# Kernel tuning notes

Hardware: AMD Instinct MI355X
Metric: run time of the kernel (lower is better)

Reference implementation:

```python
import jax, jax.numpy as jnp
import numpy as np

TEMPERATURE = 0.2
EPS = 1e-12  # matches torch F.normalize eps


def _l2_normalize(x):
    n = jnp.linalg.norm(x, axis=-1, keepdims=True)
    return x / jnp.maximum(n, EPS)


def setup_inputs() -> dict:
    key = jax.random.key(0)
    k1, k2 = jax.random.split(key)
    B, D = 8192, 256
    return {
        "user_embeddings": jax.random.normal(k1, (B, D), dtype=jnp.float32),
        "positive_item_embeddings": jax.random.normal(k2, (B, D), dtype=jnp.float32),
    }


def reference(user_embeddings, positive_item_embeddings):
    # all_item_embeddings=None branch: in-batch implicit negatives.
    u = _l2_normalize(user_embeddings)            # [B, D]
    p = _l2_normalize(positive_item_embeddings)   # [B, D]
    sim = jnp.einsum("bd,nd->bn", u, p) / TEMPERATURE  # [B, B]
    pos_sim = jnp.diagonal(sim)                   # [B]; equals the torch pos_sim
    # Original concatenates pos_sim[i] with the off-diagonal row entries and takes
    # logsumexp. Since the diagonal of sim IS pos_sim[i], that set equals the full
    # row, so loss_i = -pos_sim_i + logsumexp(sim[i, :]). Vectorized over the batch.
    lse = jax.nn.logsumexp(sim, axis=1)           # [B]
    return jnp.mean(lse - pos_sim)
```

## Files before the change

kernel.cpp:

```cpp
#include <hip/hip_runtime.h>
#include <hip/hip_bf16.h>

#define DDIM 256
#define NROWS 8192

typedef __attribute__((ext_vector_type(8))) __bf16 bf16x8;
typedef __attribute__((ext_vector_type(4))) float floatx4;

__device__ __forceinline__ void async16(const void* g, void* l) {
    __builtin_amdgcn_global_load_lds(
        (const __attribute__((address_space(1))) unsigned int*)g,
        (__attribute__((address_space(3))) unsigned int*)l,
        16, 0, 0);
}

__device__ __forceinline__ float fexp2(float x) {
    float r; asm("v_exp_f32 %0, %1" : "=v"(r) : "v"(x)); return r;
}

__global__ __launch_bounds__(256) void normalize_kernel(
    const float* __restrict__ U, const float* __restrict__ P,
    unsigned short* __restrict__ Un, unsigned short* __restrict__ Pn,
    float* __restrict__ possim, float* __restrict__ rowsum,
    float* __restrict__ out, int* __restrict__ counter)
{
    if (blockIdx.x == 0 && threadIdx.x == 0) { out[0] = 0.0f; counter[0] = 0; }
    const int lane = threadIdx.x & 63;
    const int row  = blockIdx.x * 4 + (threadIdx.x >> 6);
    const size_t base = (size_t)row * DDIM + lane * 4;
    const float4 u4 = *(const float4*)(U + base);
    const float4 p4 = *(const float4*)(P + base);
    float su = u4.x*u4.x + u4.y*u4.y + u4.z*u4.z + u4.w*u4.w;
    float sp = p4.x*p4.x + p4.y*p4.y + p4.z*p4.z + p4.w*p4.w;
    float up = u4.x*p4.x + u4.y*p4.y + u4.z*p4.z + u4.w*p4.w;
    #pragma unroll
    for (int d = 1; d < 64; d <<= 1) {
        su += __shfl_xor(su, d);
        sp += __shfl_xor(sp, d);
        up += __shfl_xor(up, d);
    }
    const float iu = rsqrtf(fmaxf(su, 1e-24f));
    const float ip = rsqrtf(fmaxf(sp, 1e-24f));
    if (lane == 0) {
        possim[row] = up * iu * ip;
        rowsum[row] = 0.0f;
    }
    union { ushort4 s4; __hip_bfloat16 h[4]; } cu, cp;
    cu.h[0] = __float2bfloat16(u4.x * iu); cu.h[1] = __float2bfloat16(u4.y * iu);
    cu.h[2] = __float2bfloat16(u4.z * iu); cu.h[3] = __float2bfloat16(u4.w * iu);
    cp.h[0] = __float2bfloat16(p4.x * ip); cp.h[1] = __float2bfloat16(p4.y * ip);
    cp.h[2] = __float2bfloat16(p4.z * ip); cp.h[3] = __float2bfloat16(p4.w * ip);
    *(ushort4*)(Un + base) = cu.s4;
    *(ushort4*)(Pn + base) = cp.s4;
}

__device__ __forceinline__ void stage8(const unsigned short* __restrict__ g,
                                       unsigned short* l, int wv, int lane)
{
    const int lrow = lane >> 5;
    const int gcol = lane & 31;
    const int r0 = wv * 8;
    #pragma unroll
    for (int j = 0; j < 4; ++j) {
        const int rb = r0 + j * 2;
        const int r  = rb + lrow;
        const int gg = gcol ^ (r & 7);
        async16(g + (size_t)r * DDIM + gg * 8, l + (size_t)rb * DDIM);
    }
}

__global__ __launch_bounds__(512, 2) void sim_exp_rowsum(
    const unsigned short* __restrict__ Un,
    const unsigned short* __restrict__ Pn,
    float* __restrict__ rowsum,
    const float* __restrict__ possim,
    int* __restrict__ counter,
    float* __restrict__ out)
{
    __shared__ __align__(16) unsigned short lds[65536];
    __shared__ float ws8[8];
    __shared__ int ticket_s;

    const int tid  = threadIdx.x;
    const int lane = tid & 63;
    const int wv   = tid >> 6;
    const int m = lane & 15;
    const int q = lane >> 4;

    const int stripe = blockIdx.x >> 3;
    const int oct    = blockIdx.x & 7;

    const unsigned short* Arow = Un + (size_t)(stripe * 256 + wv * 32 + m) * DDIM;
    bf16x8 afr[2][8];
    #pragma unroll
    for (int t = 0; t < 2; ++t)
        #pragma unroll
        for (int ks = 0; ks < 8; ++ks)
            afr[t][ks] = *(const bf16x8*)(Arow + t * 16 * DDIM + (ks * 4 + q) * 8);

    const int c10 = m & 3, c2 = (m >> 2) & 1;
    const unsigned bb0 = (unsigned)(m * 512 + ((q ^ c10) << 4) + ((0 ^ c2) << 6));
    const unsigned bb1 = (unsigned)(m * 512 + ((q ^ c10) << 4) + ((1 ^ c2) << 6));

    const unsigned short* Bglob = Pn + (size_t)(oct * 1024) * DDIM;
    float rowpart[2][4] = {{0.f, 0.f, 0.f, 0.f}, {0.f, 0.f, 0.f, 0.f}};

    stage8(Bglob,                  lds,         wv, lane);
    stage8(Bglob + 64 * DDIM,      lds + 16384, wv, lane);
    stage8(Bglob + 128 * DDIM,     lds + 32768, wv, lane);
    asm volatile("s_waitcnt vmcnt(0)" ::: "memory");
    __builtin_amdgcn_s_barrier();

#define LOADPH(BP, P, F)                                                     \
    do {                                                                     \
        F[0] = *(const bf16x8*)((BP) + bb0 + 0 * 8192 + (P) * 128);          \
        F[1] = *(const bf16x8*)((BP) + bb0 + 1 * 8192 + (P) * 128);          \
        F[2] = *(const bf16x8*)((BP) + bb0 + 2 * 8192 + (P) * 128);          \
        F[3] = *(const bf16x8*)((BP) + bb0 + 3 * 8192 + (P) * 128);          \
        F[4] = *(const bf16x8*)((BP) + bb1 + 0 * 8192 + (P) * 128);          \
        F[5] = *(const bf16x8*)((BP) + bb1 + 1 * 8192 + (P) * 128);          \
        F[6] = *(const bf16x8*)((BP) + bb1 + 2 * 8192 + (P) * 128);          \
        F[7] = *(const bf16x8*)((BP) + bb1 + 3 * 8192 + (P) * 128);          \
    } while (0)

#define MMAPH(P, F)                                                          \
    do {                                                                     \
        __builtin_amdgcn_s_setprio(1);                                       \
        _Pragma("unroll")                                                    \
        for (int n = 0; n < 4; ++n) {                                        \
            acc[0][n] = __builtin_amdgcn_mfma_f32_16x16x32_bf16(             \
                afr[0][2 * (P)], F[n], acc[0][n], 0, 0, 0);                  \
            acc[1][n] = __builtin_amdgcn_mfma_f32_16x16x32_bf16(             \
                afr[1][2 * (P)], F[n], acc[1][n], 0, 0, 0);                  \
            acc[0][n] = __builtin_amdgcn_mfma_f32_16x16x32_bf16(             \
                afr[0][2 * (P) + 1], F[n + 4], acc[0][n], 0, 0, 0);          \
            acc[1][n] = __builtin_amdgcn_mfma_f32_16x16x32_bf16(             \
                afr[1][2 * (P) + 1], F[n + 4], acc[1][n], 0, 0, 0);          \
        }                                                                    \
        __builtin_amdgcn_s_setprio(0);                                       \
    } while (0)

    for (int i = 0; i < 16; ++i) {
        if (i > 0) {
            if (i <= 13)      asm volatile("s_waitcnt vmcnt(8)" ::: "memory");
            else if (i == 14) asm volatile("s_waitcnt vmcnt(4)" ::: "memory");
            else              asm volatile("s_waitcnt vmcnt(0)" ::: "memory");
            __builtin_amdgcn_s_barrier();
        }
        if (i + 3 < 16)
            stage8(Bglob + (size_t)(i + 3) * 64 * DDIM,
                   lds + ((i + 3) & 3) * 16384, wv, lane);

        const char* Bp = (const char*)lds + (i & 3) * 32768;
        floatx4 acc[2][4];
        #pragma unroll
        for (int t = 0; t < 2; ++t)
            #pragma unroll
            for (int n = 0; n < 4; ++n)
                acc[t][n] = {0.0f, 0.0f, 0.0f, 0.0f};

        bf16x8 fA[8], fB[8];
        LOADPH(Bp, 0, fA);
        LOADPH(Bp, 1, fB);
        MMAPH(0, fA);
        LOADPH(Bp, 2, fA);
        MMAPH(1, fB);
        LOADPH(Bp, 3, fB);
        MMAPH(2, fA);
        MMAPH(3, fB);

        #pragma unroll
        for (int t = 0; t < 2; ++t)
            #pragma unroll
            for (int n = 0; n < 4; ++n)
                #pragma unroll
                for (int r = 0; r < 4; ++r)
                    rowpart[t][r] += fexp2(acc[t][n][r] * 7.2134752044448169f);
    }
#undef LOADPH
#undef MMAPH

    #pragma unroll
    for (int t = 0; t < 2; ++t) {
        #pragma unroll
        for (int r = 0; r < 4; ++r) {
            float s = rowpart[t][r];
            s += __shfl_xor(s, 1);
            s += __shfl_xor(s, 2);
            s += __shfl_xor(s, 4);
            s += __shfl_xor(s, 8);
            if (m == 0) {
                const int grow = stripe * 256 + wv * 32 + t * 16 + q * 4 + r;
                atomicAdd(&rowsum[grow], s);
            }
        }
    }

    __threadfence();
    __syncthreads();
    if (tid == 0)
        ticket_s = __hip_atomic_fetch_add(counter, 1, __ATOMIC_ACQ_REL,
                                          __HIP_MEMORY_SCOPE_AGENT);
    __syncthreads();
    if (ticket_s == 255) {
        float part = 0.0f;
        for (int i = tid; i < NROWS; i += 512) {
            const float rs = __hip_atomic_load(&rowsum[i], __ATOMIC_RELAXED,
                                               __HIP_MEMORY_SCOPE_AGENT);
            part += __logf(rs) - 5.0f * possim[i];
        }
        #pragma unroll
        for (int d = 1; d < 64; d <<= 1) part += __shfl_xor(part, d);
        if (lane == 0) ws8[wv] = part;
        __syncthreads();
        if (tid == 0) {
            float tot = 0.0f;
            #pragma unroll
            for (int w = 0; w < 8; ++w) tot += ws8[w];
            out[0] = tot * (1.0f / (float)NROWS);
        }
    }
}

extern "C" void kernel_launch(void* const* d_in, const int* in_sizes, int n_in,
                              void* d_out, int out_size, void* d_ws, size_t ws_size,
                              hipStream_t stream) {
    const float* U = (const float*)d_in[0];
    const float* P = (const float*)d_in[1];
    float* out = (float*)d_out;
    char* ws = (char*)d_ws;
    unsigned short* Un = (unsigned short*)ws;
    unsigned short* Pn = (unsigned short*)(ws + 4194304);
    float* rowsum = (float*)(ws + 8388608);
    float* possim = (float*)(ws + 8388608 + 32768);
    int* counter  = (int*)(ws + 8388608 + 65536);

    normalize_kernel<<<NROWS / 4, 256, 0, stream>>>(U, P, Un, Pn, possim, rowsum,
                                                    out, counter);
    sim_exp_rowsum<<<256, 512, 0, stream>>>(Un, Pn, rowsum, possim, counter, out);
}
```

Measured before the change: 144.6 us.

## Fuse normalization and similarity kernels into one cooperative kernel with grid sync

Moves the L2-normalize / bf16-convert / positive-similarity pass into the start of the main similarity kernel. Each of the 256 blocks normalizes 32 rows, then a cooperative grid-wide sync runs before the tiled bf16 matmul with its exp/rowsum reduction. This removes the second kernel launch and the gap between the two kernels. In exchange it adds a grid barrier and cooperative-launch overhead, and the normalize phase now runs on fewer, larger blocks.

```diff
diff --git a/kernel.cpp b/kernel.cpp
--- a/kernel.cpp
+++ b/kernel.cpp
@@ -1,5 +1,8 @@
 #include <hip/hip_runtime.h>
 #include <hip/hip_bf16.h>
+#include <hip/hip_cooperative_groups.h>
+
+namespace cg = cooperative_groups;
 
 #define DDIM 256
 #define NROWS 8192
@@ -16,42 +19,6 @@
 
 __device__ __forceinline__ float fexp2(float x) {
     float r; asm("v_exp_f32 %0, %1" : "=v"(r) : "v"(x)); return r;
-}
-
-__global__ __launch_bounds__(256) void normalize_kernel(
-    const float* __restrict__ U, const float* __restrict__ P,
-    unsigned short* __restrict__ Un, unsigned short* __restrict__ Pn,
-    float* __restrict__ possim, float* __restrict__ rowsum,
-    float* __restrict__ out, int* __restrict__ counter)
-{
-    if (blockIdx.x == 0 && threadIdx.x == 0) { out[0] = 0.0f; counter[0] = 0; }
-    const int lane = threadIdx.x & 63;
-    const int row  = blockIdx.x * 4 + (threadIdx.x >> 6);
-    const size_t base = (size_t)row * DDIM + lane * 4;
-    const float4 u4 = *(const float4*)(U + base);
-    const float4 p4 = *(const float4*)(P + base);
-    float su = u4.x*u4.x + u4.y*u4.y + u4.z*u4.z + u4.w*u4.w;
-    float sp = p4.x*p4.x + p4.y*p4.y + p4.z*p4.z + p4.w*p4.w;
-    float up = u4.x*p4.x + u4.y*p4.y + u4.z*p4.z + u4.w*p4.w;
-    #pragma unroll
-    for (int d = 1; d < 64; d <<= 1) {
-        su += __shfl_xor(su, d);
-        sp += __shfl_xor(sp, d);
-        up += __shfl_xor(up, d);
-    }
-    const float iu = rsqrtf(fmaxf(su, 1e-24f));
-    const float ip = rsqrtf(fmaxf(sp, 1e-24f));
-    if (lane == 0) {
-        possim[row] = up * iu * ip;
-        rowsum[row] = 0.0f;
-    }
-    union { ushort4 s4; __hip_bfloat16 h[4]; } cu, cp;
-    cu.h[0] = __float2bfloat16(u4.x * iu); cu.h[1] = __float2bfloat16(u4.y * iu);
-    cu.h[2] = __float2bfloat16(u4.z * iu); cu.h[3] = __float2bfloat16(u4.w * iu);
-    cp.h[0] = __float2bfloat16(p4.x * ip); cp.h[1] = __float2bfloat16(p4.y * ip);
-    cp.h[2] = __float2bfloat16(p4.z * ip); cp.h[3] = __float2bfloat16(p4.w * ip);
-    *(ushort4*)(Un + base) = cu.s4;
-    *(ushort4*)(Pn + base) = cp.s4;
 }
 
 __device__ __forceinline__ void stage8(const unsigned short* __restrict__ g,
@@ -69,13 +36,11 @@
     }
 }
 
-__global__ __launch_bounds__(512, 2) void sim_exp_rowsum(
-    const unsigned short* __restrict__ Un,
-    const unsigned short* __restrict__ Pn,
-    float* __restrict__ rowsum,
-    const float* __restrict__ possim,
-    int* __restrict__ counter,
-    float* __restrict__ out)
+__global__ __launch_bounds__(512, 2) void fused_loss(
+    const float* __restrict__ U, const float* __restrict__ P,
+    unsigned short* __restrict__ Un, unsigned short* __restrict__ Pn,
+    float* __restrict__ rowsum, float* __restrict__ possim,
+    int* __restrict__ counter, float* __restrict__ out)
 {
     __shared__ __align__(16) unsigned short lds[65536];
     __shared__ float ws8[8];
@@ -87,6 +52,44 @@
     const int m = lane & 15;
     const int q = lane >> 4;
 
+    if (blockIdx.x == 0 && tid == 0) counter[0] = 0;
+    {
+        const int r0 = blockIdx.x * 32 + wv * 4;
+        #pragma unroll
+        for (int rr = 0; rr < 4; ++rr) {
+            const int row = r0 + rr;
+            const size_t base = (size_t)row * DDIM + lane * 4;
+            const float4 u4 = *(const float4*)(U + base);
+            const float4 p4 = *(const float4*)(P + base);
+            float su = u4.x*u4.x + u4.y*u4.y + u4.z*u4.z + u4.w*u4.w;
+            float sp = p4.x*p4.x + p4.y*p4.y + p4.z*p4.z + p4.w*p4.w;
+            float up = u4.x*p4.x + u4.y*p4.y + u4.z*p4.z + u4.w*p4.w;
+            #pragma unroll
+            for (int d = 1; d < 64; d <<= 1) {
+                su += __shfl_xor(su, d);
+                sp += __shfl_xor(sp, d);
+                up += __shfl_xor(up, d);
+            }
+            const float iu = rsqrtf(fmaxf(su, 1e-24f));
+            const float ip = rsqrtf(fmaxf(sp, 1e-24f));
+            if (lane == 0) possim[row] = up * iu * ip;
+            union { ushort4 s4; __hip_bfloat16 h[4]; } cu, cp;
+            cu.h[0] = __float2bfloat16(u4.x * iu);
+            cu.h[1] = __float2bfloat16(u4.y * iu);
+            cu.h[2] = __float2bfloat16(u4.z * iu);
+            cu.h[3] = __float2bfloat16(u4.w * iu);
+            cp.h[0] = __float2bfloat16(p4.x * ip);
+            cp.h[1] = __float2bfloat16(p4.y * ip);
+            cp.h[2] = __float2bfloat16(p4.z * ip);
+            cp.h[3] = __float2bfloat16(p4.w * ip);
+            *(ushort4*)(Un + base) = cu.s4;
+            *(ushort4*)(Pn + base) = cp.s4;
+        }
+        if (tid < 32) rowsum[blockIdx.x * 32 + tid] = 0.0f;
+    }
+
+    cg::this_grid().sync();
+
     const int stripe = blockIdx.x >> 3;
     const int oct    = blockIdx.x & 7;
 
@@ -105,9 +108,9 @@
     const unsigned short* Bglob = Pn + (size_t)(oct * 1024) * DDIM;
     float rowpart[2][4] = {{0.f, 0.f, 0.f, 0.f}, {0.f, 0.f, 0.f, 0.f}};
 
-    stage8(Bglob,                  lds,         wv, lane);
-    stage8(Bglob + 64 * DDIM,      lds + 16384, wv, lane);
-    stage8(Bglob + 128 * DDIM,     lds + 32768, wv, lane);
+    stage8(Bglob,              lds,         wv, lane);
+    stage8(Bglob + 64 * DDIM,  lds + 16384, wv, lane);
+    stage8(Bglob + 128 * DDIM, lds + 32768, wv, lane);
     asm volatile("s_waitcnt vmcnt(0)" ::: "memory");
     __builtin_amdgcn_s_barrier();
 
@@ -235,7 +238,8 @@
     float* possim = (float*)(ws + 8388608 + 32768);
     int* counter  = (int*)(ws + 8388608 + 65536);
 
-    normalize_kernel<<<NROWS / 4, 256, 0, stream>>>(U, P, Un, Pn, possim, rowsum,
-                                                    out, counter);
-    sim_exp_rowsum<<<256, 512, 0, stream>>>(Un, Pn, rowsum, possim, counter, out);
-}
+    void* args[] = {(void*)&U, (void*)&P, (void*)&Un, (void*)&Pn,
+                    (void*)&rowsum, (void*)&possim, (void*)&counter, (void*)&out};
+    hipLaunchCooperativeKernel((const void*)fused_loss, dim3(256), dim3(512),
+                               args, 0, stream);
+}
```

Result: slower. 186.3 us (+28.9%).

## Load B fragments directly from global memory instead of staging through LDS

Applied to the files above, without the earlier changes.

Removes the LDS staging ring buffer, the async global-to-LDS copies and the per-iteration barriers. Each wave now reads its B fragments straight from global memory into registers, software-pipelined one phase ahead across iterations. This drops LDS traffic and block-wide synchronisation, but every wave independently fetches the same B tile. That multiplies global/L2 reads and exposes global latency to the MFMA loop.

```diff
diff --git a/kernel.cpp b/kernel.cpp
--- a/kernel.cpp
+++ b/kernel.cpp
@@ -6,13 +6,6 @@
 
 typedef __attribute__((ext_vector_type(8))) __bf16 bf16x8;
 typedef __attribute__((ext_vector_type(4))) float floatx4;
-
-__device__ __forceinline__ void async16(const void* g, void* l) {
-    __builtin_amdgcn_global_load_lds(
-        (const __attribute__((address_space(1))) unsigned int*)g,
-        (__attribute__((address_space(3))) unsigned int*)l,
-        16, 0, 0);
-}
 
 __device__ __forceinline__ float fexp2(float x) {
     float r; asm("v_exp_f32 %0, %1" : "=v"(r) : "v"(x)); return r;
@@ -54,21 +47,6 @@
     *(ushort4*)(Pn + base) = cp.s4;
 }
 
-__device__ __forceinline__ void stage8(const unsigned short* __restrict__ g,
-                                       unsigned short* l, int wv, int lane)
-{
-    const int lrow = lane >> 5;
-    const int gcol = lane & 31;
-    const int r0 = wv * 8;
-    #pragma unroll
-    for (int j = 0; j < 4; ++j) {
-        const int rb = r0 + j * 2;
-        const int r  = rb + lrow;
-        const int gg = gcol ^ (r & 7);
-        async16(g + (size_t)r * DDIM + gg * 8, l + (size_t)rb * DDIM);
-    }
-}
-
 __global__ __launch_bounds__(512, 2) void sim_exp_rowsum(
     const unsigned short* __restrict__ Un,
     const unsigned short* __restrict__ Pn,
@@ -77,7 +55,6 @@
     int* __restrict__ counter,
     float* __restrict__ out)
 {
-    __shared__ __align__(16) unsigned short lds[65536];
     __shared__ float ws8[8];
     __shared__ int ticket_s;
 
@@ -98,29 +75,24 @@
         for (int ks = 0; ks < 8; ++ks)
             afr[t][ks] = *(const bf16x8*)(Arow + t * 16 * DDIM + (ks * 4 + q) * 8);
 
-    const int c10 = m & 3, c2 = (m >> 2) & 1;
-    const unsigned bb0 = (unsigned)(m * 512 + ((q ^ c10) << 4) + ((0 ^ c2) << 6));
-    const unsigned bb1 = (unsigned)(m * 512 + ((q ^ c10) << 4) + ((1 ^ c2) << 6));
-
-    const unsigned short* Bglob = Pn + (size_t)(oct * 1024) * DDIM;
+    unsigned voff[2][4];
+    #pragma unroll
+    for (int par = 0; par < 2; ++par)
+        #pragma unroll
+        for (int n = 0; n < 4; ++n)
+            voff[par][n] = (unsigned)((n * 16 + m) * 512 + q * 16 + par * 64);
+
+    const char* Bbase = (const char*)(Pn + (size_t)(oct * 1024) * DDIM);
     float rowpart[2][4] = {{0.f, 0.f, 0.f, 0.f}, {0.f, 0.f, 0.f, 0.f}};
 
-    stage8(Bglob,                  lds,         wv, lane);
-    stage8(Bglob + 64 * DDIM,      lds + 16384, wv, lane);
-    stage8(Bglob + 128 * DDIM,     lds + 32768, wv, lane);
-    asm volatile("s_waitcnt vmcnt(0)" ::: "memory");
-    __builtin_amdgcn_s_barrier();
-
-#define LOADPH(BP, P, F)                                                     \
+#define LOADG(BS, P, F)                                                      \
     do {                                                                     \
-        F[0] = *(const bf16x8*)((BP) + bb0 + 0 * 8192 + (P) * 128);          \
-        F[1] = *(const bf16x8*)((BP) + bb0 + 1 * 8192 + (P) * 128);          \
-        F[2] = *(const bf16x8*)((BP) + bb0 + 2 * 8192 + (P) * 128);          \
-        F[3] = *(const bf16x8*)((BP) + bb0 + 3 * 8192 + (P) * 128);          \
-        F[4] = *(const bf16x8*)((BP) + bb1 + 0 * 8192 + (P) * 128);          \
-        F[5] = *(const bf16x8*)((BP) + bb1 + 1 * 8192 + (P) * 128);          \
-        F[6] = *(const bf16x8*)((BP) + bb1 + 2 * 8192 + (P) * 128);          \
-        F[7] = *(const bf16x8*)((BP) + bb1 + 3 * 8192 + (P) * 128);          \
+        _Pragma("unroll")                                                    \
+        for (int par = 0; par < 2; ++par)                                    \
+            _Pragma("unroll")                                                \
+            for (int n = 0; n < 4; ++n)                                      \
+                F[par * 4 + n] = *(const bf16x8*)((BS) + voff[par][n]        \
+                                                  + (P) * 128);              \
     } while (0)
 
 #define MMAPH(P, F)                                                          \
@@ -140,18 +112,13 @@
         __builtin_amdgcn_s_setprio(0);                                       \
     } while (0)
 
+    bf16x8 fA[8], fB[8];
+    LOADG(Bbase, 0, fA);
+    LOADG(Bbase, 1, fB);
+
     for (int i = 0; i < 16; ++i) {
-        if (i > 0) {
-            if (i <= 13)      asm volatile("s_waitcnt vmcnt(8)" ::: "memory");
-            else if (i == 14) asm volatile("s_waitcnt vmcnt(4)" ::: "memory");
-            else              asm volatile("s_waitcnt vmcnt(0)" ::: "memory");
-            __builtin_amdgcn_s_barrier();
-        }
-        if (i + 3 < 16)
-            stage8(Bglob + (size_t)(i + 3) * 64 * DDIM,
-                   lds + ((i + 3) & 3) * 16384, wv, lane);
-
-        const char* Bp = (const char*)lds + (i & 3) * 32768;
+        const char* Bs  = Bbase + (unsigned)i * 32768u;
+        const char* Bsn = Bs + 32768u;
         floatx4 acc[2][4];
         #pragma unroll
         for (int t = 0; t < 2; ++t)
@@ -159,15 +126,10 @@
             for (int n = 0; n < 4; ++n)
                 acc[t][n] = {0.0f, 0.0f, 0.0f, 0.0f};
 
-        bf16x8 fA[8], fB[8];
-        LOADPH(Bp, 0, fA);
-        LOADPH(Bp, 1, fB);
-        MMAPH(0, fA);
-        LOADPH(Bp, 2, fA);
-        MMAPH(1, fB);
-        LOADPH(Bp, 3, fB);
-        MMAPH(2, fA);
-        MMAPH(3, fB);
+        MMAPH(0, fA);  LOADG(Bs, 2, fA);
+        MMAPH(1, fB);  LOADG(Bs, 3, fB);
+        MMAPH(2, fA);  if (i < 15) LOADG(Bsn, 0, fA);
+        MMAPH(3, fB);  if (i < 15) LOADG(Bsn, 1, fB);
 
         #pragma unroll
         for (int t = 0; t < 2; ++t)
@@ -177,7 +139,7 @@
                 for (int r = 0; r < 4; ++r)
                     rowpart[t][r] += fexp2(acc[t][n][r] * 7.2134752044448169f);
     }
-#undef LOADPH
+#undef LOADG
 #undef MMAPH
 
     #pragma unroll
```

Measured after the change: 214.4 us. 48.3% more time.

## Interleave async B staging with per-phase MFMA and barrier-synchronized LDS reads

Applied to the files above, without the earlier changes.

Replaces the bulk stage8 prefetch per iteration with four async global-to-LDS loads spread across the four k-phases, each issued alongside that phase's LDS fragment reads. Each phase is bracketed by workgroup barriers and an lgkmcnt wait, so all waves load, then compute together at raised priority. This also drops the double-buffered fA/fB register overlap in favour of a single fragment set. The aim is to spread memory traffic evenly and keep waves in lockstep, at the cost of eight extra barriers per iteration and less overlap between LDS reads and MFMA.

```diff
diff --git a/kernel.cpp b/kernel.cpp
--- a/kernel.cpp
+++ b/kernel.cpp
@@ -102,12 +102,21 @@
     const unsigned bb0 = (unsigned)(m * 512 + ((q ^ c10) << 4) + ((0 ^ c2) << 6));
     const unsigned bb1 = (unsigned)(m * 512 + ((q ^ c10) << 4) + ((1 ^ c2) << 6));
 
+    const int lrow = lane >> 5, gcol = lane & 31;
+    unsigned soff[4];
+    #pragma unroll
+    for (int j = 0; j < 4; ++j) {
+        const int r = wv * 8 + j * 2 + lrow;
+        const int gg = gcol ^ (r & 7);
+        soff[j] = (unsigned)(r * 512 + gg * 16);
+    }
+
     const unsigned short* Bglob = Pn + (size_t)(oct * 1024) * DDIM;
     float rowpart[2][4] = {{0.f, 0.f, 0.f, 0.f}, {0.f, 0.f, 0.f, 0.f}};
 
-    stage8(Bglob,                  lds,         wv, lane);
-    stage8(Bglob + 64 * DDIM,      lds + 16384, wv, lane);
-    stage8(Bglob + 128 * DDIM,     lds + 32768, wv, lane);
+    stage8(Bglob,              lds,         wv, lane);
+    stage8(Bglob + 64 * DDIM,  lds + 16384, wv, lane);
+    stage8(Bglob + 128 * DDIM, lds + 32768, wv, lane);
     asm volatile("s_waitcnt vmcnt(0)" ::: "memory");
     __builtin_amdgcn_s_barrier();
 
@@ -125,7 +134,6 @@
 
 #define MMAPH(P, F)                                                          \
     do {                                                                     \
-        __builtin_amdgcn_s_setprio(1);                                       \
         _Pragma("unroll")                                                    \
         for (int n = 0; n < 4; ++n) {                                        \
             acc[0][n] = __builtin_amdgcn_mfma_f32_16x16x32_bf16(             \
@@ -137,7 +145,6 @@
             acc[1][n] = __builtin_amdgcn_mfma_f32_16x16x32_bf16(             \
                 afr[1][2 * (P) + 1], F[n + 4], acc[1][n], 0, 0, 0);          \
         }                                                                    \
-        __builtin_amdgcn_s_setprio(0);                                       \
     } while (0)
 
     for (int i = 0; i < 16; ++i) {
@@ -147,11 +154,12 @@
             else              asm volatile("s_waitcnt vmcnt(0)" ::: "memory");
             __builtin_amdgcn_s_barrier();
         }
-        if (i + 3 < 16)
-            stage8(Bglob + (size_t)(i + 3) * 64 * DDIM,
-                   lds + ((i + 3) & 3) * 16384, wv, lane);
 
         const char* Bp = (const char*)lds + (i & 3) * 32768;
+        const bool do_stage = (i + 3 < 16);
+        const unsigned short* sg = Bglob + (size_t)(i + 3) * 64 * DDIM;
+        unsigned short* sl = lds + ((i + 3) & 3) * 16384 + wv * 2048;
+
         floatx4 acc[2][4];
         #pragma unroll
         for (int t = 0; t < 2; ++t)
@@ -159,15 +167,23 @@
             for (int n = 0; n < 4; ++n)
                 acc[t][n] = {0.0f, 0.0f, 0.0f, 0.0f};
 
-        bf16x8 fA[8], fB[8];
-        LOADPH(Bp, 0, fA);
-        LOADPH(Bp, 1, fB);
-        MMAPH(0, fA);
-        LOADPH(Bp, 2, fA);
-        MMAPH(1, fB);
-        LOADPH(Bp, 3, fB);
-        MMAPH(2, fA);
-        MMAPH(3, fB);
+        bf16x8 F[8];
+        #pragma unroll
+        for (int p = 0; p < 4; ++p) {
+            LOADPH(Bp, p, F);
+            if (do_stage)
+                async16((const char*)sg + soff[p],
+                        (char*)sl + p * 1024);
+            __builtin_amdgcn_sched_barrier(0);
+            __builtin_amdgcn_s_barrier();
+            asm volatile("s_waitcnt lgkmcnt(0)" ::: "memory");
+            __builtin_amdgcn_sched_barrier(0);
+            __builtin_amdgcn_s_setprio(1);
+            MMAPH(p, F);
+            __builtin_amdgcn_s_setprio(0);
+            __builtin_amdgcn_sched_barrier(0);
+            __builtin_amdgcn_s_barrier();
+        }
 
         #pragma unroll
         for (int t = 0; t < 2; ++t)
```

After: 146.8 us. About the same (+1.6%).
